# Kernel tuning notes

Measured on AMD Instinct MI355X. Metric: run time of the kernel, lower is better.

Reference implementation:

```python
import jax, jax.numpy as jnp
import numpy as np

B = 16          # number of point clouds (equal-sized, contiguous batch ids)
NC_PER = 1024   # coarse points per cloud
NF_PER = 4096   # fine points per cloud
K = 3           # knn_interpolate neighbors
C_IN = 512      # coarse feature channels
C_SKIP = 256    # skip feature channels
C_OUT = 512
BN_EPS = 1e-5


def setup_inputs() -> dict:
    key = jax.random.key(0)
    ks = jax.random.split(key, 8)
    Nc, Nf = B * NC_PER, B * NF_PER
    d_in = C_IN + C_SKIP
    x = jax.random.normal(ks[0], (Nc, C_IN), jnp.float32)
    pos = jax.random.uniform(ks[1], (Nc, 3), jnp.float32)
    batch = jnp.repeat(jnp.arange(B, dtype=jnp.int64), NC_PER)
    x_skip = jax.random.normal(ks[2], (Nf, C_SKIP), jnp.float32)
    pos_skip = jax.random.uniform(ks[3], (Nf, 3), jnp.float32)
    batch_skip = jnp.repeat(jnp.arange(B, dtype=jnp.int64), NF_PER)
    W1 = jax.random.normal(ks[4], (d_in, C_OUT), jnp.float32) / np.sqrt(d_in)
    W2 = jax.random.normal(ks[5], (C_OUT, C_OUT), jnp.float32) / np.sqrt(C_OUT)
    return {
        "x": x, "pos": pos, "batch": batch,
        "x_skip": x_skip, "pos_skip": pos_skip, "batch_skip": batch_skip,
        "W1": W1, "b1": jnp.zeros((C_OUT,), jnp.float32),
        "g1": jnp.ones((C_OUT,), jnp.float32), "be1": jnp.zeros((C_OUT,), jnp.float32),
        "W2": W2, "b2": jnp.zeros((C_OUT,), jnp.float32),
        "g2": jnp.ones((C_OUT,), jnp.float32), "be2": jnp.zeros((C_OUT,), jnp.float32),
    }


def _knn_interpolate(x, pos, pos_skip):
    # batches are contiguous and equal-sized -> reshape to [B, n, .] (honors batch/batch_skip)
    xb = x.reshape(B, NC_PER, C_IN)
    pc = pos.reshape(B, NC_PER, 3)
    pf = pos_skip.reshape(B, NF_PER, 3)
    # squared pairwise distances [B, NF_PER, NC_PER] via ||a||^2 + ||b||^2 - 2ab
    d2 = ((pf * pf).sum(-1)[:, :, None]
          + (pc * pc).sum(-1)[:, None, :]
          - 2.0 * jnp.einsum('bfd,bcd->bfc', pf, pc))
    neg_d2, idx = jax.lax.top_k(-d2, K)           # [B, NF_PER, K]
    w = 1.0 / jnp.maximum(-neg_d2, 1e-16)         # inverse squared-distance weights
    gathered = jax.vmap(lambda xi, ii: xi[ii])(xb, idx)   # [B, NF_PER, K, C_IN]
    y = (w[..., None] * gathered).sum(2) / w.sum(2)[..., None]
    return y.reshape(B * NF_PER, C_IN)


def _bn_act(h, g, be):
    # BatchNorm1d in training mode (biased variance) + ReLU
    mu = h.mean(0)
    var = ((h - mu) ** 2).mean(0)
    return jax.nn.relu((h - mu) * jax.lax.rsqrt(var + BN_EPS) * g + be)


def reference(x, pos, batch, x_skip, pos_skip, batch_skip,
              W1, b1, g1, be1, W2, b2, g2, be2):
    xi = _knn_interpolate(x, pos, pos_skip)        # [Nf, C_IN]
    h = jnp.concatenate([xi, x_skip], axis=1)      # [Nf, C_IN + C_SKIP]
    h = _bn_act(h @ W1 + b1, g1, be1)
    h = _bn_act(h @ W2 + b2, g2, be2)
    return (h, pos_skip, batch_skip)
```

## Files before the change

### kernel.cpp

```cpp
#include <hip/hip_runtime.h>
#include <cstdint>
#include <cstddef>

#define BATCHES   16
#define NC_PER    1024
#define NF_PER    4096
#define NC_TOT    (BATCHES * NC_PER)
#define NF_TOT    (BATCHES * NF_PER)
#define C_IN      512
#define C_SKIP    256
#define D_IN      (C_IN + C_SKIP)
#define C_OUT     512
#define BN_EPS    1e-5f

typedef __bf16 bf16x8 __attribute__((ext_vector_type(8)));
typedef __bf16 bf16x4 __attribute__((ext_vector_type(4)));
typedef float  f32x4  __attribute__((ext_vector_type(4)));

static_assert(sizeof(__bf16) == 2, "bf16 size");

__global__ __launch_bounds__(256) void transpose_to_bf16(
    const float* __restrict__ W, __bf16* __restrict__ Wt, int K, int N) {
  int idx = blockIdx.x * 256 + threadIdx.x;
  if (idx >= K * N) return;
  int n = idx / K;
  int k = idx - n * K;
  Wt[idx] = (__bf16)W[k * N + n];
}

__global__ __launch_bounds__(256) void knn_kernel(
    const float* __restrict__ pos,
    const float* __restrict__ pos_skip,
    int4*  __restrict__ idx3,
    float4* __restrict__ w3)
{
  __shared__ float s_pos[NC_PER * 3];
  __shared__ float s_pc2[NC_PER];
  __shared__ float s_pd[4][64][3];
  __shared__ int   s_pi[4][64][3];

  const int tid   = threadIdx.x;
  const int bi    = blockIdx.x;
  const int fbase = bi * 64;
  const int b     = fbase >> 12;
  const int cbase = b * NC_PER;

  for (int i = tid; i < NC_PER * 3; i += 256)
    s_pos[i] = pos[(size_t)cbase * 3 + i];
  __syncthreads();
  for (int j = tid; j < NC_PER; j += 256) {
    float cx = s_pos[j * 3 + 0], cy = s_pos[j * 3 + 1], cz = s_pos[j * 3 + 2];
    s_pc2[j] = __fadd_rn(__fadd_rn(__fmul_rn(cx, cx), __fmul_rn(cy, cy)),
                         __fmul_rn(cz, cz));
  }
  __syncthreads();

  const int p   = tid & 63;
  const int seg = tid >> 6;
  const int f   = fbase + p;
  const float px = pos_skip[f * 3 + 0];
  const float py = pos_skip[f * 3 + 1];
  const float pz = pos_skip[f * 3 + 2];
  const float pf2 = __fadd_rn(__fadd_rn(__fmul_rn(px, px), __fmul_rn(py, py)),
                              __fmul_rn(pz, pz));
  float b0 = 1e30f, b1 = 1e30f, b2 = 1e30f;
  int   i0 = 0,     i1 = 0,     i2 = 0;
  const int j0 = seg * 256;
#pragma unroll 4
  for (int jj = 0; jj < 256; ++jj) {
    const int j = j0 + jj;
    float cx = s_pos[j * 3 + 0], cy = s_pos[j * 3 + 1], cz = s_pos[j * 3 + 2];
    float dot = __fadd_rn(__fadd_rn(__fmul_rn(px, cx), __fmul_rn(py, cy)),
                          __fmul_rn(pz, cz));
    float d2 = __fsub_rn(__fadd_rn(pf2, s_pc2[j]), __fmul_rn(2.0f, dot));
    if (d2 < b2) {
      if (d2 < b1) {
        b2 = b1; i2 = i1;
        if (d2 < b0) { b1 = b0; i1 = i0; b0 = d2; i0 = j; }
        else         { b1 = d2; i1 = j; }
      } else { b2 = d2; i2 = j; }
    }
  }
  s_pd[seg][p][0] = b0; s_pd[seg][p][1] = b1; s_pd[seg][p][2] = b2;
  s_pi[seg][p][0] = i0; s_pi[seg][p][1] = i1; s_pi[seg][p][2] = i2;
  __syncthreads();

  if (tid < 64) {
    float m0 = 1e30f, m1 = 1e30f, m2 = 1e30f;
    int  mi0 = 0,    mi1 = 0,    mi2 = 0;
#pragma unroll
    for (int s = 0; s < 4; ++s)
#pragma unroll
      for (int k = 0; k < 3; ++k) {
        float d = s_pd[s][tid][k];
        int   i = s_pi[s][tid][k];
        if (d < m2 || (d == m2 && i < mi2)) {
          if (d < m1 || (d == m1 && i < mi1)) {
            m2 = m1; mi2 = mi1;
            if (d < m0 || (d == m0 && i < mi0)) {
              m1 = m0; mi1 = mi0; m0 = d; mi0 = i;
            } else { m1 = d; mi1 = i; }
          } else { m2 = d; mi2 = i; }
        }
      }
    float w0 = 1.0f / fmaxf(m0, 1e-16f);
    float w1 = 1.0f / fmaxf(m1, 1e-16f);
    float w2 = 1.0f / fmaxf(m2, 1e-16f);
    float inv = 1.0f / __fadd_rn(__fadd_rn(w0, w1), w2);
    const int fo = fbase + tid;
    idx3[fo] = make_int4(mi0, mi1, mi2, 0);
    w3[fo]   = make_float4(w0 * inv, w1 * inv, w2 * inv, 0.f);
  }
}

__global__ __launch_bounds__(256) void gather_interp(
    const float* __restrict__ x,
    const float* __restrict__ x_skip,
    const int4*  __restrict__ idx3,
    const float4* __restrict__ w3,
    __bf16* __restrict__ h0)
{
  const int bi   = blockIdx.x;
  const int xcd  = bi & 7;
  const int slot = bi >> 3;
  const int batch = xcd * 2 + (slot >> 10);
  const int blk   = slot & 1023;
  const int wv = threadIdx.x >> 6, ln = threadIdx.x & 63;
  const int f = batch * NF_PER + blk * 4 + wv;
  const int cbase = batch * NC_PER;

  const int4   id = idx3[f];
  const float4 w  = w3[f];
  const float* x0 = x + (size_t)(cbase + id.x) * C_IN;
  const float* x1 = x + (size_t)(cbase + id.y) * C_IN;
  const float* x2 = x + (size_t)(cbase + id.z) * C_IN;
  __bf16* o = h0 + (size_t)f * D_IN;
  const int c0 = ln * 4;
#pragma unroll
  for (int it = 0; it < 2; ++it) {
    const int c = c0 + it * 256;
    float4 a0 = *(const float4*)(x0 + c);
    float4 a1 = *(const float4*)(x1 + c);
    float4 a2 = *(const float4*)(x2 + c);
    bf16x4 ov;
    ov[0] = (__bf16)(w.x * a0.x + w.y * a1.x + w.z * a2.x);
    ov[1] = (__bf16)(w.x * a0.y + w.y * a1.y + w.z * a2.y);
    ov[2] = (__bf16)(w.x * a0.z + w.y * a1.z + w.z * a2.z);
    ov[3] = (__bf16)(w.x * a0.w + w.y * a1.w + w.z * a2.w);
    *(bf16x4*)(o + c) = ov;
  }
  float4 s = *(const float4*)(x_skip + (size_t)f * C_SKIP + c0);
  bf16x4 sv;
  sv[0] = (__bf16)s.x; sv[1] = (__bf16)s.y;
  sv[2] = (__bf16)s.z; sv[3] = (__bf16)s.w;
  *(bf16x4*)(o + C_IN + c0) = sv;
}

template <int K, bool BF16OUT>
__global__ __launch_bounds__(256) void gemm_bt(
    const __bf16* __restrict__ A,
    const __bf16* __restrict__ Bt,
    const float*  __restrict__ bias,
    void* __restrict__ Cout,
    float* __restrict__ part1)
{
  __shared__ __align__(16) __bf16 As[128 * 32];
  __shared__ __align__(16) __bf16 Bs[128 * 32];
  __shared__ float s_red[2][4][16][2];

  const int tid  = threadIdx.x;
  const int wave = tid >> 6, lane = tid & 63;
  const int quad = lane >> 4, l16 = lane & 15;
  const int wm = wave >> 1, wn = wave & 1;
  const int m0 = blockIdx.y * 128, n0 = blockIdx.x * 128;

  f32x4 acc[4][4] = {};

  for (int k0 = 0; k0 < K; k0 += 32) {
    __syncthreads();
#pragma unroll
    for (int q = 0; q < 2; ++q) {
      const int chunk = q * 256 + wave * 64 + lane;
      const int row = chunk >> 2;
      const int col = (chunk & 3) << 3;
      __builtin_amdgcn_global_load_lds(
          (const __attribute__((address_space(1))) unsigned int*)(A + (size_t)(m0 + row) * K + (k0 + col)),
          (__attribute__((address_space(3))) unsigned int*)(As + (q * 256 + wave * 64) * 8),
          16, 0, 0);
      __builtin_amdgcn_global_load_lds(
          (const __attribute__((address_space(1))) unsigned int*)(Bt + (size_t)(n0 + row) * K + (k0 + col)),
          (__attribute__((address_space(3))) unsigned int*)(Bs + (q * 256 + wave * 64) * 8),
          16, 0, 0);
    }
    __syncthreads();

    bf16x8 af[4], bfv[4];
#pragma unroll
    for (int t = 0; t < 4; ++t) {
      af[t]  = *(const bf16x8*)&As[(wm * 64 + t * 16 + l16) * 32 + quad * 8];
      bfv[t] = *(const bf16x8*)&Bs[(wn * 64 + t * 16 + l16) * 32 + quad * 8];
    }
#pragma unroll
    for (int tm = 0; tm < 4; ++tm)
#pragma unroll
      for (int tn = 0; tn < 4; ++tn)
        acc[tm][tn] = __builtin_amdgcn_mfma_f32_16x16x32_bf16(
            af[tm], bfv[tn], acc[tm][tn], 0, 0, 0);
  }

  float sArr[4], ssArr[4];
#pragma unroll
  for (int tn = 0; tn < 4; ++tn) {
    const int n = n0 + wn * 64 + tn * 16 + l16;
    const float bv = bias[n];
    float s = 0.f, ss = 0.f;
#pragma unroll
    for (int tm = 0; tm < 4; ++tm) {
      const int mb = m0 + wm * 64 + tm * 16 + quad * 4;
#pragma unroll
      for (int r = 0; r < 4; ++r) {
        const float v = acc[tm][tn][r] + bv;
        s += v; ss += v * v;
        if constexpr (BF16OUT)
          ((__bf16*)Cout)[(size_t)(mb + r) * 512 + n] = (__bf16)v;
        else
          ((float*)Cout)[(size_t)(mb + r) * 512 + n] = v;
      }
    }
    s  += __shfl_down(s, 32);  s  += __shfl_down(s, 16);
    ss += __shfl_down(ss, 32); ss += __shfl_down(ss, 16);
    sArr[tn] = s; ssArr[tn] = ss;
  }
  if (wm == 1 && quad == 0) {
#pragma unroll
    for (int tn = 0; tn < 4; ++tn) {
      s_red[wn][tn][l16][0] = sArr[tn];
      s_red[wn][tn][l16][1] = ssArr[tn];
    }
  }
  __syncthreads();
  if (wm == 0 && quad == 0) {
    float* row = part1 + (size_t)blockIdx.y * 1024;
#pragma unroll
    for (int tn = 0; tn < 4; ++tn) {
      const int n = n0 + wn * 64 + tn * 16 + l16;
      row[n]       = sArr[tn]  + s_red[wn][tn][l16][0];
      row[512 + n] = ssArr[tn] + s_red[wn][tn][l16][1];
    }
  }
}

__global__ __launch_bounds__(256) void reduce_partials(
    const float* __restrict__ part1, float* __restrict__ part2) {
  const int rb = blockIdx.x;
  const int t  = threadIdx.x;
#pragma unroll
  for (int k = 0; k < 4; ++k) {
    const int c = k * 256 + t;
    float acc = 0.f;
    const float* p = part1 + (size_t)rb * 32 * 1024 + c;
#pragma unroll 8
    for (int r = 0; r < 32; ++r) { acc += *p; p += 1024; }
    part2[rb * 1024 + c] = acc;
  }
}

__global__ void finalize_stats(const float* __restrict__ part2,
                               const float* __restrict__ g,
                               const float* __restrict__ be,
                               float* __restrict__ ab, float invM) {
  const int c = blockIdx.x * 256 + threadIdx.x;
  if (c < 512) {
    float s = 0.f, ss = 0.f;
#pragma unroll
    for (int r = 0; r < 16; ++r) {
      s  += part2[r * 1024 + c];
      ss += part2[r * 1024 + 512 + c];
    }
    float mean = s * invM;
    float var  = ss * invM - mean * mean;
    float a = g[c] * rsqrtf(var + BN_EPS);
    ab[c] = a;
    ab[512 + c] = be[c] - mean * a;
  }
}

__global__ __launch_bounds__(256) void bnrelu_bf16(
    __bf16* __restrict__ H, const float* __restrict__ ab) {
  const size_t e = ((size_t)blockIdx.x * 256 + threadIdx.x) * 4;
  const int c = (int)(e & 511);
  bf16x4* p = (bf16x4*)(H + e);
  bf16x4 h = *p;
#pragma unroll
  for (int i = 0; i < 4; ++i) {
    float v = (float)h[i];
    v = fmaxf(fmaf(v, ab[c + i], ab[512 + c + i]), 0.f);
    h[i] = (__bf16)v;
  }
  *p = h;
}

__global__ __launch_bounds__(256) void bnrelu_b2f(
    const __bf16* __restrict__ H, const float* __restrict__ ab,
    float* __restrict__ O) {
  const size_t e = ((size_t)blockIdx.x * 256 + threadIdx.x) * 4;
  const int c = (int)(e & 511);
  bf16x4 h = *(const bf16x4*)(H + e);
  float4 o;
  o.x = fmaxf(fmaf((float)h[0], ab[c + 0], ab[512 + c + 0]), 0.f);
  o.y = fmaxf(fmaf((float)h[1], ab[c + 1], ab[512 + c + 1]), 0.f);
  o.z = fmaxf(fmaf((float)h[2], ab[c + 2], ab[512 + c + 2]), 0.f);
  o.w = fmaxf(fmaf((float)h[3], ab[c + 3], ab[512 + c + 3]), 0.f);
  *(float4*)(O + e) = o;
}

__global__ __launch_bounds__(256) void tail_kernel(
    const float* __restrict__ pos_skip, float* __restrict__ out2) {
  const int i = blockIdx.x * 256 + threadIdx.x;
  if (i < NF_TOT * 3) {
    out2[i] = pos_skip[i];
  } else {
    const int f = i - NF_TOT * 3;
    out2[i] = (float)(f >> 12);
  }
}

extern "C" void kernel_launch(void* const* d_in, const int* in_sizes, int n_in,
                              void* d_out, int out_size, void* d_ws, size_t ws_size,
                              hipStream_t stream) {
  (void)in_sizes; (void)n_in; (void)out_size; (void)ws_size;

  const float* x        = (const float*)d_in[0];
  const float* pos      = (const float*)d_in[1];
  const float* x_skip   = (const float*)d_in[3];
  const float* pos_skip = (const float*)d_in[4];
  const float* W1  = (const float*)d_in[6];
  const float* b1  = (const float*)d_in[7];
  const float* g1  = (const float*)d_in[8];
  const float* be1 = (const float*)d_in[9];
  const float* W2  = (const float*)d_in[10];
  const float* b2  = (const float*)d_in[11];
  const float* g2  = (const float*)d_in[12];
  const float* be2 = (const float*)d_in[13];
  float* out = (float*)d_out;

  char* ws = (char*)d_ws;
  __bf16* h0   = (__bf16*)(ws);
  __bf16* h2   = (__bf16*)(ws);
  __bf16* h1   = (__bf16*)(ws + 100663296ull);
  __bf16* W1t  = (__bf16*)(ws + 167772160ull);
  __bf16* W2t  = (__bf16*)(ws + 168558592ull);
  float*  ab1   = (float*)(ws + 169086976ull);
  float*  ab2   = (float*)(ws + 169095168ull);
  int4*   idx3  = (int4*)(ws + 169099264ull);
  float4* w3    = (float4*)(ws + 170147840ull);
  float*  part1 = (float*)(ws + 169099264ull);
  float*  part2 = (float*)(ws + 171196416ull);

  transpose_to_bf16<<<(D_IN * C_OUT + 255) / 256, 256, 0, stream>>>(W1, W1t, D_IN, C_OUT);
  transpose_to_bf16<<<(C_OUT * C_OUT + 255) / 256, 256, 0, stream>>>(W2, W2t, C_OUT, C_OUT);

  knn_kernel<<<NF_TOT / 64, 256, 0, stream>>>(pos, pos_skip, idx3, w3);
  gather_interp<<<NF_TOT / 4, 256, 0, stream>>>(x, x_skip, idx3, w3, h0);

  gemm_bt<D_IN, true><<<dim3(4, 512), 256, 0, stream>>>(h0, W1t, b1, (void*)h1, part1);
  reduce_partials<<<16, 256, 0, stream>>>(part1, part2);
  finalize_stats<<<2, 256, 0, stream>>>(part2, g1, be1, ab1, 1.0f / (float)NF_TOT);
  bnrelu_bf16<<<(NF_TOT * 512 / 4) / 256, 256, 0, stream>>>(h1, ab1);

  gemm_bt<C_OUT, true><<<dim3(4, 512), 256, 0, stream>>>(h1, W2t, b2, (void*)h2, part1);
  reduce_partials<<<16, 256, 0, stream>>>(part1, part2);
  finalize_stats<<<2, 256, 0, stream>>>(part2, g2, be2, ab2, 1.0f / (float)NF_TOT);
  bnrelu_b2f<<<(NF_TOT * 512 / 4) / 256, 256, 0, stream>>>(h2, ab2, out);

  tail_kernel<<<(NF_TOT * 3 + NF_TOT + 255) / 256, 256, 0, stream>>>(
      pos_skip, out + (size_t)NF_TOT * 512);
}
```

Measured before the change: 529.5 us.

## Double-buffer GEMM LDS tiles and remap blocks for XCD-aware scheduling

```diff
diff --git a/kernel.cpp b/kernel.cpp
--- a/kernel.cpp
+++ b/kernel.cpp
@@ -164,20 +164,24 @@
     void* __restrict__ Cout,
     float* __restrict__ part1)
 {
-  __shared__ __align__(16) __bf16 As[128 * 32];
-  __shared__ __align__(16) __bf16 Bs[128 * 32];
+  __shared__ __align__(16) __bf16 As[2][128 * 32];
+  __shared__ __align__(16) __bf16 Bs[2][128 * 32];
   __shared__ float s_red[2][4][16][2];
 
   const int tid  = threadIdx.x;
   const int wave = tid >> 6, lane = tid & 63;
   const int quad = lane >> 4, l16 = lane & 15;
   const int wm = wave >> 1, wn = wave & 1;
-  const int m0 = blockIdx.y * 128, n0 = blockIdx.x * 128;
+
+  const int bid  = blockIdx.x;
+  const int work = (bid & 7) * 256 + (bid >> 3);
+  const int my   = work >> 2;
+  const int nx   = work & 3;
+  const int m0 = my * 128, n0 = nx * 128;
 
   f32x4 acc[4][4] = {};
 
-  for (int k0 = 0; k0 < K; k0 += 32) {
-    __syncthreads();
+  auto stage = [&](int buf, int k0) {
 #pragma unroll
     for (int q = 0; q < 2; ++q) {
       const int chunk = q * 256 + wave * 64 + lane;
@@ -185,20 +189,27 @@
       const int col = (chunk & 3) << 3;
       __builtin_amdgcn_global_load_lds(
           (const __attribute__((address_space(1))) unsigned int*)(A + (size_t)(m0 + row) * K + (k0 + col)),
-          (__attribute__((address_space(3))) unsigned int*)(As + (q * 256 + wave * 64) * 8),
+          (__attribute__((address_space(3))) unsigned int*)(As[buf] + (q * 256 + wave * 64) * 8),
           16, 0, 0);
       __builtin_amdgcn_global_load_lds(
           (const __attribute__((address_space(1))) unsigned int*)(Bt + (size_t)(n0 + row) * K + (k0 + col)),
-          (__attribute__((address_space(3))) unsigned int*)(Bs + (q * 256 + wave * 64) * 8),
+          (__attribute__((address_space(3))) unsigned int*)(Bs[buf] + (q * 256 + wave * 64) * 8),
           16, 0, 0);
     }
-    __syncthreads();
+  };
+
+  stage(0, 0);
+  __syncthreads();
+
+  int cur = 0;
+  for (int k0 = 0; k0 < K; k0 += 32) {
+    if (k0 + 32 < K) stage(cur ^ 1, k0 + 32);
 
     bf16x8 af[4], bfv[4];
 #pragma unroll
     for (int t = 0; t < 4; ++t) {
-      af[t]  = *(const bf16x8*)&As[(wm * 64 + t * 16 + l16) * 32 + quad * 8];
-      bfv[t] = *(const bf16x8*)&Bs[(wn * 64 + t * 16 + l16) * 32 + quad * 8];
+      af[t]  = *(const bf16x8*)&As[cur][(wm * 64 + t * 16 + l16) * 32 + quad * 8];
+      bfv[t] = *(const bf16x8*)&Bs[cur][(wn * 64 + t * 16 + l16) * 32 + quad * 8];
     }
 #pragma unroll
     for (int tm = 0; tm < 4; ++tm)
@@ -206,6 +217,9 @@
       for (int tn = 0; tn < 4; ++tn)
         acc[tm][tn] = __builtin_amdgcn_mfma_f32_16x16x32_bf16(
             af[tm], bfv[tn], acc[tm][tn], 0, 0, 0);
+
+    __syncthreads();
+    cur ^= 1;
   }
 
   float sArr[4], ssArr[4];
@@ -240,7 +254,7 @@
   }
   __syncthreads();
   if (wm == 0 && quad == 0) {
-    float* row = part1 + (size_t)blockIdx.y * 1024;
+    float* row = part1 + (size_t)my * 1024;
 #pragma unroll
     for (int tn = 0; tn < 4; ++tn) {
       const int n = n0 + wn * 64 + tn * 16 + l16;
@@ -363,12 +377,12 @@
   knn_kernel<<<NF_TOT / 64, 256, 0, stream>>>(pos, pos_skip, idx3, w3);
   gather_interp<<<NF_TOT / 4, 256, 0, stream>>>(x, x_skip, idx3, w3, h0);
 
-  gemm_bt<D_IN, true><<<dim3(4, 512), 256, 0, stream>>>(h0, W1t, b1, (void*)h1, part1);
+  gemm_bt<D_IN, true><<<2048, 256, 0, stream>>>(h0, W1t, b1, (void*)h1, part1);
   reduce_partials<<<16, 256, 0, stream>>>(part1, part2);
   finalize_stats<<<2, 256, 0, stream>>>(part2, g1, be1, ab1, 1.0f / (float)NF_TOT);
   bnrelu_bf16<<<(NF_TOT * 512 / 4) / 256, 256, 0, stream>>>(h1, ab1);
 
-  gemm_bt<C_OUT, true><<<dim3(4, 512), 256, 0, stream>>>(h1, W2t, b2, (void*)h2, part1);
+  gemm_bt<C_OUT, true><<<2048, 256, 0, stream>>>(h1, W2t, b2, (void*)h2, part1);
   reduce_partials<<<16, 256, 0, stream>>>(part1, part2);
   finalize_stats<<<2, 256, 0, stream>>>(part2, g2, be2, ab2, 1.0f / (float)NF_TOT);
   bnrelu_b2f<<<(NF_TOT * 512 / 4) / 256, 256, 0, stream>>>(h2, ab2, out);
```

After: 522.5 us. About the same (-1.3%).

## Rewrite bf16 GEMM with 256x256 tiles, double-buffered LDS and swizzled loads

Applied to the files above, without the earlier changes.

```diff
diff --git a/kernel.cpp b/kernel.cpp
--- a/kernel.cpp
+++ b/kernel.cpp
@@ -157,69 +157,161 @@
 }
 
 template <int K, bool BF16OUT>
-__global__ __launch_bounds__(256) void gemm_bt(
+__global__ __launch_bounds__(512, 2) void gemm_bt(
     const __bf16* __restrict__ A,
     const __bf16* __restrict__ Bt,
     const float*  __restrict__ bias,
     void* __restrict__ Cout,
     float* __restrict__ part1)
 {
-  __shared__ __align__(16) __bf16 As[128 * 32];
-  __shared__ __align__(16) __bf16 Bs[128 * 32];
-  __shared__ float s_red[2][4][16][2];
+  constexpr int NT = K / 64;
+  __shared__ __align__(16) __bf16 As[2 * 16384];
+  __shared__ __align__(16) __bf16 Bs[2 * 16384];
+  __shared__ float s_red[4][4][16][2];
 
   const int tid  = threadIdx.x;
   const int wave = tid >> 6, lane = tid & 63;
   const int quad = lane >> 4, l16 = lane & 15;
-  const int wm = wave >> 1, wn = wave & 1;
-  const int m0 = blockIdx.y * 128, n0 = blockIdx.x * 128;
-
-  f32x4 acc[4][4] = {};
-
-  for (int k0 = 0; k0 < K; k0 += 32) {
-    __syncthreads();
+  const int wm = wave >> 2, wn = wave & 3;
+
+  const int bid  = blockIdx.x;
+  const int work = (bid & 7) * 64 + (bid >> 3);
+  const int mt = work >> 1, nt = work & 1;
+  const int m0 = mt * 256, n0 = nt * 256;
+
+  const int rowA = wave * 8 + (lane >> 3);
+  const int kOff = ((lane & 7) ^ (lane >> 3)) * 8;
+  const int ldsChunkBase = (wave * 64) * 8;
+
+  auto stage_half = [&](const __bf16* __restrict__ src, int rowBase, int t,
+                        __bf16* dst) {
 #pragma unroll
     for (int q = 0; q < 2; ++q) {
-      const int chunk = q * 256 + wave * 64 + lane;
-      const int row = chunk >> 2;
-      const int col = (chunk & 3) << 3;
       __builtin_amdgcn_global_load_lds(
-          (const __attribute__((address_space(1))) unsigned int*)(A + (size_t)(m0 + row) * K + (k0 + col)),
-          (__attribute__((address_space(3))) unsigned int*)(As + (q * 256 + wave * 64) * 8),
+          (const __attribute__((address_space(1))) unsigned int*)(
+              src + (size_t)(rowBase + q * 64 + rowA) * K + t * 64 + kOff),
+          (__attribute__((address_space(3))) unsigned int*)(
+              dst + q * 4096 + ldsChunkBase),
           16, 0, 0);
-      __builtin_amdgcn_global_load_lds(
-          (const __attribute__((address_space(1))) unsigned int*)(Bt + (size_t)(n0 + row) * K + (k0 + col)),
-          (__attribute__((address_space(3))) unsigned int*)(Bs + (q * 256 + wave * 64) * 8),
-          16, 0, 0);
-    }
-    __syncthreads();
-
-    bf16x8 af[4], bfv[4];
-#pragma unroll
-    for (int t = 0; t < 4; ++t) {
-      af[t]  = *(const bf16x8*)&As[(wm * 64 + t * 16 + l16) * 32 + quad * 8];
-      bfv[t] = *(const bf16x8*)&Bs[(wn * 64 + t * 16 + l16) * 32 + quad * 8];
-    }
-#pragma unroll
-    for (int tm = 0; tm < 4; ++tm)
-#pragma unroll
-      for (int tn = 0; tn < 4; ++tn)
-        acc[tm][tn] = __builtin_amdgcn_mfma_f32_16x16x32_bf16(
-            af[tm], bfv[tn], acc[tm][tn], 0, 0, 0);
+    }
+  };
+
+  f32x4 acc[8][4] = {};
+  const int swz  = (l16 & 7) << 3;
+  const int brow = (wn & 1) * 64;
+
+  stage_half(A,  m0,       0, As);
+  stage_half(Bt, n0,       0, Bs);
+  stage_half(A,  m0 + 128, 0, As + 8192);
+  stage_half(Bt, n0 + 128, 0, Bs + 8192);
+
+  bf16x8 aA[4][2], bB[4][2];
+#pragma unroll 2
+  for (int t = 0; t < NT; ++t) {
+    const int cur = t & 1;
+    const __bf16* Ab = As + (cur * 2 + wm) * 8192;
+    const __bf16* Bb = Bs + (cur * 2 + (wn >> 1)) * 8192;
+    __bf16* Asn = As + (cur ^ 1) * 16384;
+    __bf16* Bsn = Bs + (cur ^ 1) * 16384;
+
+    if (t + 1 < NT) {
+      stage_half(A,  m0,       t + 1, Asn);
+      stage_half(Bt, n0,       t + 1, Bsn);
+      asm volatile("s_waitcnt vmcnt(4)" ::: "memory");
+    } else {
+      asm volatile("s_waitcnt vmcnt(0)" ::: "memory");
+    }
+    __builtin_amdgcn_sched_barrier(0);
+    __builtin_amdgcn_s_barrier();
+#pragma unroll
+    for (int mf = 0; mf < 4; ++mf)
+#pragma unroll
+      for (int ks = 0; ks < 2; ++ks)
+        aA[mf][ks] = *(const bf16x8*)(Ab + (mf * 16 + l16) * 64 +
+                                      ((ks * 32 + quad * 8) ^ swz));
+#pragma unroll
+    for (int nf = 0; nf < 2; ++nf)
+#pragma unroll
+      for (int ks = 0; ks < 2; ++ks)
+        bB[nf][ks] = *(const bf16x8*)(Bb + (brow + nf * 16 + l16) * 64 +
+                                      ((ks * 32 + quad * 8) ^ swz));
+    __builtin_amdgcn_s_setprio(1);
+#pragma unroll
+    for (int mf = 0; mf < 4; ++mf)
+#pragma unroll
+      for (int nf = 0; nf < 2; ++nf)
+#pragma unroll
+        for (int ks = 0; ks < 2; ++ks)
+          acc[mf][nf] = __builtin_amdgcn_mfma_f32_16x16x32_bf16(
+              aA[mf][ks], bB[nf][ks], acc[mf][nf], 0, 0, 0);
+    __builtin_amdgcn_s_setprio(0);
+    __builtin_amdgcn_s_barrier();
+
+    if (t + 1 < NT) {
+      stage_half(A,  m0 + 128, t + 1, Asn + 8192);
+      stage_half(Bt, n0 + 128, t + 1, Bsn + 8192);
+    }
+#pragma unroll
+    for (int nf = 2; nf < 4; ++nf)
+#pragma unroll
+      for (int ks = 0; ks < 2; ++ks)
+        bB[nf][ks] = *(const bf16x8*)(Bb + (brow + nf * 16 + l16) * 64 +
+                                      ((ks * 32 + quad * 8) ^ swz));
+    __builtin_amdgcn_s_setprio(1);
+#pragma unroll
+    for (int mf = 0; mf < 4; ++mf)
+#pragma unroll
+      for (int nf = 2; nf < 4; ++nf)
+#pragma unroll
+        for (int ks = 0; ks < 2; ++ks)
+          acc[mf][nf] = __builtin_amdgcn_mfma_f32_16x16x32_bf16(
+              aA[mf][ks], bB[nf][ks], acc[mf][nf], 0, 0, 0);
+    __builtin_amdgcn_s_setprio(0);
+    __builtin_amdgcn_s_barrier();
+
+#pragma unroll
+    for (int mf = 0; mf < 4; ++mf)
+#pragma unroll
+      for (int ks = 0; ks < 2; ++ks)
+        aA[mf][ks] = *(const bf16x8*)(Ab + (64 + mf * 16 + l16) * 64 +
+                                      ((ks * 32 + quad * 8) ^ swz));
+    __builtin_amdgcn_s_setprio(1);
+#pragma unroll
+    for (int mf = 0; mf < 4; ++mf)
+#pragma unroll
+      for (int nf = 0; nf < 2; ++nf)
+#pragma unroll
+        for (int ks = 0; ks < 2; ++ks)
+          acc[4 + mf][nf] = __builtin_amdgcn_mfma_f32_16x16x32_bf16(
+              aA[mf][ks], bB[nf][ks], acc[4 + mf][nf], 0, 0, 0);
+    __builtin_amdgcn_s_setprio(0);
+    __builtin_amdgcn_s_barrier();
+
+    __builtin_amdgcn_s_setprio(1);
+#pragma unroll
+    for (int mf = 0; mf < 4; ++mf)
+#pragma unroll
+      for (int nf = 2; nf < 4; ++nf)
+#pragma unroll
+        for (int ks = 0; ks < 2; ++ks)
+          acc[4 + mf][nf] = __builtin_amdgcn_mfma_f32_16x16x32_bf16(
+              aA[mf][ks], bB[nf][ks], acc[4 + mf][nf], 0, 0, 0);
+    __builtin_amdgcn_s_setprio(0);
+    __builtin_amdgcn_s_barrier();
   }
 
   float sArr[4], ssArr[4];
 #pragma unroll
-  for (int tn = 0; tn < 4; ++tn) {
-    const int n = n0 + wn * 64 + tn * 16 + l16;
+  for (int nf = 0; nf < 4; ++nf) {
+    const int n = n0 + wn * 64 + nf * 16 + l16;
     const float bv = bias[n];
     float s = 0.f, ss = 0.f;
 #pragma unroll
-    for (int tm = 0; tm < 4; ++tm) {
-      const int mb = m0 + wm * 64 + tm * 16 + quad * 4;
+    for (int mf = 0; mf < 8; ++mf) {
+      const int mb = m0 + wm * 128 + mf * 16 + quad * 4;
 #pragma unroll
       for (int r = 0; r < 4; ++r) {
-        const float v = acc[tm][tn][r] + bv;
+        const float v = acc[mf][nf][r] + bv;
         s += v; ss += v * v;
         if constexpr (BF16OUT)
           ((__bf16*)Cout)[(size_t)(mb + r) * 512 + n] = (__bf16)v;
@@ -229,23 +321,24 @@
     }
     s  += __shfl_down(s, 32);  s  += __shfl_down(s, 16);
     ss += __shfl_down(ss, 32); ss += __shfl_down(ss, 16);
-    sArr[tn] = s; ssArr[tn] = ss;
+    sArr[nf] = s; ssArr[nf] = ss;
   }
   if (wm == 1 && quad == 0) {
 #pragma unroll
-    for (int tn = 0; tn < 4; ++tn) {
-      s_red[wn][tn][l16][0] = sArr[tn];
-      s_red[wn][tn][l16][1] = ssArr[tn];
-    }
-  }
-  __syncthreads();
+    for (int nf = 0; nf < 4; ++nf) {
+      s_red[wn][nf][l16][0] = sArr[nf];
+      s_red[wn][nf][l16][1] = ssArr[nf];
+    }
+  }
+  asm volatile("s_waitcnt lgkmcnt(0)" ::: "memory");
+  __builtin_amdgcn_s_barrier();
   if (wm == 0 && quad == 0) {
-    float* row = part1 + (size_t)blockIdx.y * 1024;
-#pragma unroll
-    for (int tn = 0; tn < 4; ++tn) {
-      const int n = n0 + wn * 64 + tn * 16 + l16;
-      row[n]       = sArr[tn]  + s_red[wn][tn][l16][0];
-      row[512 + n] = ssArr[tn] + s_red[wn][tn][l16][1];
+    float* row = part1 + (size_t)mt * 1024;
+#pragma unroll
+    for (int nf = 0; nf < 4; ++nf) {
+      const int n = n0 + wn * 64 + nf * 16 + l16;
+      row[n]       = sArr[nf]  + s_red[wn][nf][l16][0];
+      row[512 + n] = ssArr[nf] + s_red[wn][nf][l16][1];
     }
   }
 }
@@ -258,9 +351,9 @@
   for (int k = 0; k < 4; ++k) {
     const int c = k * 256 + t;
     float acc = 0.f;
-    const float* p = part1 + (size_t)rb * 32 * 1024 + c;
-#pragma unroll 8
-    for (int r = 0; r < 32; ++r) { acc += *p; p += 1024; }
+    const float* p = part1 + (size_t)rb * 16 * 1024 + c;
+#pragma unroll
+    for (int r = 0; r < 16; ++r) { acc += *p; p += 1024; }
     part2[rb * 1024 + c] = acc;
   }
 }
@@ -363,12 +456,12 @@
   knn_kernel<<<NF_TOT / 64, 256, 0, stream>>>(pos, pos_skip, idx3, w3);
   gather_interp<<<NF_TOT / 4, 256, 0, stream>>>(x, x_skip, idx3, w3, h0);
 
-  gemm_bt<D_IN, true><<<dim3(4, 512), 256, 0, stream>>>(h0, W1t, b1, (void*)h1, part1);
+  gemm_bt<D_IN, true><<<512, 512, 0, stream>>>(h0, W1t, b1, (void*)h1, part1);
   reduce_partials<<<16, 256, 0, stream>>>(part1, part2);
   finalize_stats<<<2, 256, 0, stream>>>(part2, g1, be1, ab1, 1.0f / (float)NF_TOT);
   bnrelu_bf16<<<(NF_TOT * 512 / 4) / 256, 256, 0, stream>>>(h1, ab1);
 
-  gemm_bt<C_OUT, true><<<dim3(4, 512), 256, 0, stream>>>(h1, W2t, b2, (void*)h2, part1);
+  gemm_bt<C_OUT, true><<<512, 512, 0, stream>>>(h1, W2t, b2, (void*)h2, part1);
   reduce_partials<<<16, 256, 0, stream>>>(part1, part2);
   finalize_stats<<<2, 256, 0, stream>>>(part2, g2, be2, ab2, 1.0f / (float)NF_TOT);
   bnrelu_b2f<<<(NF_TOT * 512 / 4) / 256, 256, 0, stream>>>(h2, ab2, out);
```

After: 506.4 us. -4.4%, faster.
